# Kernel optimization log

Measured on AMD Instinct MI355X. Metric: run time of the kernel, lower is better.

## Reference

```python
import jax, jax.numpy as jnp
import numpy as np

N = 12        # ALL_QUBITS
COM_Q = 9     # COM_QUBITS
IMG_Q = 11    # IMG_QUBITS
LAYERS = 2
SQRT2 = float(np.sqrt(2.0))
H_GATE = jnp.asarray([[1.0, 1.0], [1.0, -1.0]], dtype=jnp.complex64) / SQRT2


def _bitrev_perm(q):
    # column j of the wires-1..q subspace corresponds to param index bitrev(j)
    idx = np.arange(2 ** q)
    rev = np.zeros_like(idx)
    for bpos in range(q):
        rev |= ((idx >> bpos) & 1) << (q - 1 - bpos)
    return rev


def _apply_1q(state, U, w):
    # state: (B, 2^N) complex; apply 2x2 gate U on wire w (wire 0 = MSB)
    B = state.shape[0]
    s = state.reshape(B, 2 ** w, 2, -1)
    return jnp.einsum('ij,bpjq->bpiq', U, s).reshape(B, -1)


def _apply_cnot(state, c, t):
    B = state.shape[0]
    s = state.reshape((B,) + (2,) * N)
    s0 = jax.lax.slice_in_dim(s, 0, 1, axis=c + 1)
    s1 = jnp.flip(jax.lax.slice_in_dim(s, 1, 2, axis=c + 1), axis=t + 1)
    return jnp.concatenate([s0, s1], axis=c + 1).reshape(B, -1)


def _frqi(state, angles, q):
    # Hadamards on wires 1..q, then uniformly-controlled RY(angles) on wire 0
    for w in range(1, q + 1):
        state = _apply_1q(state, H_GATE, w)
    rev = _bitrev_perm(q)
    half = 0.5 * angles[:, rev]            # (B, 2^q), angle per control column
    c = jnp.cos(half)[:, :, None]
    s = jnp.sin(half)[:, :, None]
    B = state.shape[0]
    st = state.reshape(B, 2, 2 ** q, -1)   # (B, wire0, wires1..q, rest)
    new0 = c * st[:, 0] - s * st[:, 1]
    new1 = s * st[:, 0] + c * st[:, 1]
    return jnp.stack([new0, new1], axis=1).reshape(B, -1)


def _rot(phi, theta, omega):
    # PennyLane Rot = RZ(omega) RY(theta) RZ(phi)
    c = jnp.cos(theta / 2)
    s = jnp.sin(theta / 2)
    m00 = jnp.exp(-0.5j * (phi + omega)) * c
    m01 = -jnp.exp(0.5j * (phi - omega)) * s
    m10 = jnp.exp(-0.5j * (phi - omega)) * s
    m11 = jnp.exp(0.5j * (phi + omega)) * c
    return jnp.stack([jnp.stack([m00, m01]), jnp.stack([m10, m11])])


def _circuit(com_params, img_params, qp):
    B = com_params.shape[0]
    state = jnp.zeros((B, 2 ** N), jnp.complex64).at[:, 0].set(1.0)
    state = _frqi(state, com_params, COM_Q)
    for l in range(LAYERS):  # StronglyEntanglingLayers
        for w in range(N):
            state = _apply_1q(state, _rot(qp[l, w, 0], qp[l, w, 1], qp[l, w, 2]), w)
        r = l % (N - 1) + 1  # default ranges
        for w in range(N):
            state = _apply_cnot(state, w, (w + r) % N)
    state = _frqi(state, img_params, IMG_Q)
    p = (jnp.abs(state.reshape(B, 2, -1)) ** 2).sum(axis=2)  # (B, 2) wire-0 probs
    return p[:, 1] - p[:, 0]  # expval of Hamiltonian = -1 * Z(0)


def setup_inputs() -> dict:
    key = jax.random.key(0)
    k1, k2, k3 = jax.random.split(key, 3)
    B = 1024
    x = jax.random.uniform(k1, (B, 2, 32, 32), dtype=jnp.float32)
    W = jax.random.normal(k2, (512, 2048), dtype=jnp.float32) * 0.02
    b = jnp.zeros((512,), dtype=jnp.float32)
    quantum_params = jax.random.uniform(k3, (LAYERS, N, 3), dtype=jnp.float32) * float(np.pi)
    return {"x": x, "W": W, "b": b, "quantum_params": quantum_params}


def reference(x, W, b, quantum_params):
    B = x.shape[0]
    xf = x.reshape(B, -1)                 # (B, 2048) img_params
    com = xf @ W.T + b                    # (B, 512) classical_nn output
    return _circuit(com, xf, quantum_params)
```

## Files before the change

kernel.cpp:

```cpp
#include <hip/hip_runtime.h>
#include <hip/hip_bf16.h>
#include <math.h>

#define RS2f 0.70710678118654752f

typedef __attribute__((ext_vector_type(8))) short bf16x8;
typedef __attribute__((ext_vector_type(4))) float f32x4;

__device__ __forceinline__ float bf2f(unsigned short h) {
    return __uint_as_float(((unsigned)h) << 16);
}
__device__ __forceinline__ ushort2 pk2(float a, float b) {
    union { __hip_bfloat162 h; ushort2 s; } u;
    u.h = __float22bfloat162_rn(make_float2(a, b));
    return u.s;
}

__global__ __launch_bounds__(256) void gemm_fused(const float* __restrict__ A,
                                                  const float* __restrict__ B,
                                                  float* __restrict__ P, int nch) {
    __shared__ short As[64 * 136];
    __shared__ short Bs[64 * 136];
    const int tid = threadIdx.x, lane = tid & 63, wv = tid >> 6;
    const int quad = lane >> 4, mrow = lane & 15;
    const int bid = blockIdx.x;
    const int xcd = bid & 7;
    const int idx = bid >> 3;
    const int mt  = ((xcd >> 1) << 2) | (idx & 3);
    const int nt  = ((xcd & 1) << 2) | ((idx >> 2) & 3);
    const int zt  = idx >> 4;
    const int m0 = mt * 64, n0 = nt * 64;
    const int kb = zt * nch * 64;
    const int srow = tid >> 2;
    const int sc = (tid & 3) * 16;

    f32x4 acc[4];
    #pragma unroll
    for (int j = 0; j < 4; ++j) acc[j] = (f32x4){0.f, 0.f, 0.f, 0.f};

    const float* Arow = A + (size_t)(m0 + srow) * 2048 + kb + sc;
    const float* Brow = B + (size_t)(n0 + srow) * 2048 + kb + sc;

    float4 av[4], bv[4];
    #pragma unroll
    for (int i = 0; i < 4; ++i) { av[i] = *(const float4*)(Arow + 4*i);
                                  bv[i] = *(const float4*)(Brow + 4*i); }

    for (int ch = 0; ch < nch; ++ch) {
        __syncthreads();
        #pragma unroll
        for (int i = 0; i < 4; ++i) {
            ushort2 h0 = pk2(av[i].x, av[i].y);
            ushort2 h1 = pk2(av[i].z, av[i].w);
            ushort2 l0 = pk2(av[i].x - bf2f(h0.x), av[i].y - bf2f(h0.y));
            ushort2 l1 = pk2(av[i].z - bf2f(h1.x), av[i].w - bf2f(h1.y));
            *(ushort4*)&As[srow * 136 + sc + 4*i]      = make_ushort4(h0.x, h0.y, h1.x, h1.y);
            *(ushort4*)&As[srow * 136 + 64 + sc + 4*i] = make_ushort4(l0.x, l0.y, l1.x, l1.y);
            h0 = pk2(bv[i].x, bv[i].y);
            h1 = pk2(bv[i].z, bv[i].w);
            l0 = pk2(bv[i].x - bf2f(h0.x), bv[i].y - bf2f(h0.y));
            l1 = pk2(bv[i].z - bf2f(h1.x), bv[i].w - bf2f(h1.y));
            *(ushort4*)&Bs[srow * 136 + sc + 4*i]      = make_ushort4(h0.x, h0.y, h1.x, h1.y);
            *(ushort4*)&Bs[srow * 136 + 64 + sc + 4*i] = make_ushort4(l0.x, l0.y, l1.x, l1.y);
        }
        __syncthreads();
        if (ch + 1 < nch) {
            const int o = (ch + 1) * 64;
            #pragma unroll
            for (int i = 0; i < 4; ++i) { av[i] = *(const float4*)(Arow + o + 4*i);
                                          bv[i] = *(const float4*)(Brow + o + 4*i); }
        }
        #pragma unroll
        for (int s = 0; s < 4; ++s) {
            const int off = s * 32 + quad * 8;
            bf16x8 af = *(const bf16x8*)&As[(wv * 16 + mrow) * 136 + off];
            #pragma unroll
            for (int j = 0; j < 4; ++j) {
                bf16x8 bf = *(const bf16x8*)&Bs[(j * 16 + mrow) * 136 + off];
                acc[j] = __builtin_amdgcn_mfma_f32_16x16x32_bf16(af, bf, acc[j], 0, 0, 0);
            }
        }
    }
    float* Pz = P + (size_t)zt * 524288;
    #pragma unroll
    for (int j = 0; j < 4; ++j)
        #pragma unroll
        for (int r = 0; r < 4; ++r)
            Pz[(m0 + wv * 16 + quad * 4 + r) * 512 + n0 + j * 16 + mrow] = acc[j][r];
}

__global__ __launch_bounds__(256) void reduce_kernel(float* __restrict__ P,
                                                     const float* __restrict__ bias,
                                                     int SK) {
    int i = blockIdx.x * 256 + threadIdx.x;
    float s = bias[i & 511];
    for (int z = 0; z < SK; ++z) s += P[(size_t)z * 524288 + i];
    P[i] = s;
}

__global__ __launch_bounds__(256) void gemm_f32(const float* __restrict__ A,
                                                const float* __restrict__ W,
                                                float* __restrict__ C) {
    __shared__ float Asf[64][33];
    __shared__ float Bsf[32][33];
    const int tid = threadIdx.x;
    const int m0 = blockIdx.x * 64;
    const int n0 = blockIdx.y * 32;
    const int tm = tid >> 4, tn = tid & 15;
    float acc[4][2] = {};
    for (int k0 = 0; k0 < 2048; k0 += 32) {
        #pragma unroll
        for (int i = 0; i < 8; ++i) {
            int idx = tid + i * 256;
            Asf[idx >> 5][idx & 31] = A[(m0 + (idx >> 5)) * 2048 + k0 + (idx & 31)];
        }
        #pragma unroll
        for (int i = 0; i < 4; ++i) {
            int idx = tid + i * 256;
            Bsf[idx >> 5][idx & 31] = W[(n0 + (idx >> 5)) * 2048 + k0 + (idx & 31)];
        }
        __syncthreads();
        #pragma unroll
        for (int kk = 0; kk < 32; ++kk) {
            float a0 = Asf[tm*4+0][kk], a1 = Asf[tm*4+1][kk];
            float a2 = Asf[tm*4+2][kk], a3 = Asf[tm*4+3][kk];
            float b0 = Bsf[tn*2+0][kk], b1 = Bsf[tn*2+1][kk];
            acc[0][0] += a0*b0; acc[0][1] += a0*b1;
            acc[1][0] += a1*b0; acc[1][1] += a1*b1;
            acc[2][0] += a2*b0; acc[2][1] += a2*b1;
            acc[3][0] += a3*b0; acc[3][1] += a3*b1;
        }
        __syncthreads();
    }
    #pragma unroll
    for (int r = 0; r < 4; ++r)
        #pragma unroll
        for (int c = 0; c < 2; ++c)
            C[(m0 + tm*4 + r) * 512 + n0 + tn*2 + c] = acc[r][c];
}

struct CMat { float m00r,m00i,m01r,m01i,m10r,m10i,m11r,m11i; };

__device__ __forceinline__ CMat mk_rot(const float* __restrict__ qp, int l, int w) {
    const float* g = qp + (l * 12 + w) * 3;
    float phi = g[0], th = g[1], om = g[2];
    float st, ct, sa, ca, sb, cb;
    sincosf(0.5f * th, &st, &ct);
    sincosf(0.5f * (phi + om), &sa, &ca);
    sincosf(0.5f * (phi - om), &sb, &cb);
    CMat M;
    M.m00r =  ct * ca; M.m00i = -ct * sa;
    M.m01r = -st * cb; M.m01i = -st * sb;
    M.m10r =  st * cb; M.m10i = -st * sb;
    M.m11r =  ct * ca; M.m11i =  ct * sa;
    return M;
}

template<int W> struct WI {
    static constexpr int kind = (W == 0 || W == 7) ? 2 : ((W >= 1 && W <= 6) ? 1 : 0);
    static constexpr int eb   = (W >= 8) ? (11 - W) : 0;
    static constexpr int lm   = (W >= 1 && W <= 6) ? (1 << (6 - W)) : 0;
    static constexpr int vm   = (W == 0) ? 2 : ((W == 7) ? 1 : 0);
};

__device__ __forceinline__ void exch_put(float* xbuf, int slot,
                                         const float vr[16], const float vi[16]) {
    __syncthreads();
    float4* p = (float4*)xbuf;
    #pragma unroll
    for (int j = 0; j < 8; ++j)
        p[(j << 8) + slot] = make_float4(vr[2*j], vi[2*j], vr[2*j+1], vi[2*j+1]);
    __syncthreads();
}

__device__ __forceinline__ void shfl_perm(float vr[16], float vi[16], int src) {
    #pragma unroll
    for (int e = 0; e < 16; ++e) {
        vr[e] = __shfl(vr[e], src, 64);
        vi[e] = __shfl(vi[e], src, 64);
    }
}

template<int EB>
__device__ __forceinline__ void rot_local(float vr[16], float vi[16], const CMat& M) {
    #pragma unroll
    for (int e = 0; e < 16; ++e) if (!(e & (1 << EB))) {
        const int e1 = e | (1 << EB);
        float x0r = vr[e],  x0i = vi[e];
        float x1r = vr[e1], x1i = vi[e1];
        vr[e]  = M.m00r*x0r - M.m00i*x0i + M.m01r*x1r - M.m01i*x1i;
        vi[e]  = M.m00r*x0i + M.m00i*x0r + M.m01r*x1i + M.m01i*x1r;
        vr[e1] = M.m10r*x0r - M.m10i*x0i + M.m11r*x1r - M.m11i*x1i;
        vi[e1] = M.m10r*x0i + M.m10i*x0r + M.m11r*x1i + M.m11i*x1r;
    }
}

template<int LM>
__device__ __forceinline__ void rot_lane(float vr[16], float vi[16], int lane, const CMat& M) {
    const bool hi = lane & LM;
    const float Ar = hi ? M.m11r : M.m00r, Ai = hi ? M.m11i : M.m00i;
    const float Br = hi ? M.m10r : M.m01r, Bi = hi ? M.m10i : M.m01i;
    #pragma unroll
    for (int e = 0; e < 16; ++e) {
        float pr = __shfl_xor(vr[e], LM, 64);
        float pi = __shfl_xor(vi[e], LM, 64);
        float orr = vr[e], oi = vi[e];
        vr[e] = Ar*orr - Ai*oi + Br*pr - Bi*pi;
        vi[e] = Ar*oi + Ai*orr + Br*pi + Bi*pr;
    }
}

template<int VM>
__device__ __forceinline__ void rot_wave(float vr[16], float vi[16], float* xbuf,
                                         int waveId, int lane, const CMat& M) {
    exch_put(xbuf, (waveId << 6) + lane, vr, vi);
    const float4* p = (const float4*)xbuf;
    const int ps = ((waveId ^ VM) << 6) + lane;
    const bool hi = waveId & VM;
    const float Ar = hi ? M.m11r : M.m00r, Ai = hi ? M.m11i : M.m00i;
    const float Br = hi ? M.m10r : M.m01r, Bi = hi ? M.m10i : M.m01i;
    #pragma unroll
    for (int j = 0; j < 8; ++j) {
        float4 q = p[(j << 8) + ps];
        const int e0 = 2*j, e1 = 2*j + 1;
        float r0 = vr[e0], i0 = vi[e0], r1 = vr[e1], i1 = vi[e1];
        vr[e0] = Ar*r0 - Ai*i0 + Br*q.x - Bi*q.y;
        vi[e0] = Ar*i0 + Ai*r0 + Br*q.y + Bi*q.x;
        vr[e1] = Ar*r1 - Ai*i1 + Br*q.z - Bi*q.w;
        vi[e1] = Ar*i1 + Ai*r1 + Br*q.w + Bi*q.z;
    }
}

template<int W>
__device__ __forceinline__ void rot_wire(float vr[16], float vi[16], float* xbuf,
                                         int waveId, int lane, const CMat& M) {
    if constexpr (WI<W>::kind == 0)      rot_local<WI<W>::eb>(vr, vi, M);
    else if constexpr (WI<W>::kind == 1) rot_lane<WI<W>::lm>(vr, vi, lane, M);
    else                                 rot_wave<WI<W>::vm>(vr, vi, xbuf, waveId, lane, M);
}

template<int C, int T>
__device__ __forceinline__ void cnot(float vr[16], float vi[16], float* xbuf,
                                     int waveId, int lane) {
    constexpr int ck = WI<C>::kind, tk = WI<T>::kind;
    if constexpr (ck == 0 && tk == 0) {
        constexpr int cb = 1 << WI<C>::eb, tb = 1 << WI<T>::eb;
        #pragma unroll
        for (int e = 0; e < 16; ++e) if ((e & cb) && !(e & tb)) {
            const int e1 = e | tb;
            float t = vr[e]; vr[e] = vr[e1]; vr[e1] = t;
            t = vi[e]; vi[e] = vi[e1]; vi[e1] = t;
        }
    } else if constexpr (ck == 0 && tk == 1) {
        constexpr int cb = 1 << WI<C>::eb, tm = WI<T>::lm;
        #pragma unroll
        for (int e = 0; e < 16; ++e) if (e & cb) {
            vr[e] = __shfl_xor(vr[e], tm, 64);
            vi[e] = __shfl_xor(vi[e], tm, 64);
        }
    } else if constexpr (ck == 0 && tk == 2) {
        constexpr int cb = 1 << WI<C>::eb, vm = WI<T>::vm;
        exch_put(xbuf, (waveId << 6) + lane, vr, vi);
        const float4* p = (const float4*)xbuf;
        const int ps = ((waveId ^ vm) << 6) + lane;
        #pragma unroll
        for (int j = 0; j < 8; ++j) {
            if ((((2*j) & cb) != 0) || (((2*j+1) & cb) != 0)) {
                float4 q = p[(j << 8) + ps];
                if (((2*j) & cb) != 0)   { vr[2*j]   = q.x; vi[2*j]   = q.y; }
                if (((2*j+1) & cb) != 0) { vr[2*j+1] = q.z; vi[2*j+1] = q.w; }
            }
        }
    } else if constexpr (ck == 1 && tk == 0) {
        constexpr int cm = WI<C>::lm, tb = 1 << WI<T>::eb;
        const bool cc = lane & cm;
        #pragma unroll
        for (int e = 0; e < 16; ++e) if (!(e & tb)) {
            const int e1 = e | tb;
            float a = vr[e], bb = vr[e1];
            vr[e] = cc ? bb : a; vr[e1] = cc ? a : bb;
            a = vi[e]; bb = vi[e1];
            vi[e] = cc ? bb : a; vi[e1] = cc ? a : bb;
        }
    } else if constexpr (ck == 1 && tk == 1) {
        constexpr int cm = WI<C>::lm, tm = WI<T>::lm;
        const int src = (lane & cm) ? (lane ^ tm) : lane;
        shfl_perm(vr, vi, src);
    } else if constexpr (ck == 1 && tk == 2) {
        constexpr int cm = WI<C>::lm, vm = WI<T>::vm;
        exch_put(xbuf, (waveId << 6) + lane, vr, vi);
        const float4* p = (const float4*)xbuf;
        const int ps = ((waveId ^ vm) << 6) + lane;
        const bool take = lane & cm;
        #pragma unroll
        for (int j = 0; j < 8; ++j) {
            float4 q = p[(j << 8) + ps];
            vr[2*j]   = take ? q.x : vr[2*j];   vi[2*j]   = take ? q.y : vi[2*j];
            vr[2*j+1] = take ? q.z : vr[2*j+1]; vi[2*j+1] = take ? q.w : vi[2*j+1];
        }
    } else if constexpr (ck == 2 && tk == 0) {
        constexpr int vm = WI<C>::vm, tb = 1 << WI<T>::eb;
        if (waveId & vm) {
            #pragma unroll
            for (int e = 0; e < 16; ++e) if (!(e & tb)) {
                const int e1 = e | tb;
                float t = vr[e]; vr[e] = vr[e1]; vr[e1] = t;
                t = vi[e]; vi[e] = vi[e1]; vi[e1] = t;
            }
        }
    } else {
        constexpr int vm = WI<C>::vm, tm = WI<T>::lm;
        if (waveId & vm) {
            #pragma unroll
            for (int e = 0; e < 16; ++e) {
                vr[e] = __shfl_xor(vr[e], tm, 64);
                vi[e] = __shfl_xor(vi[e], tm, 64);
            }
        }
    }
}

template<int W>
__device__ __forceinline__ void h_wire(float vr[16], float vi[16], float* xbuf,
                                       int waveId, int lane) {
    if constexpr (WI<W>::kind == 0) {
        constexpr int tb = 1 << WI<W>::eb;
        #pragma unroll
        for (int e = 0; e < 16; ++e) if (!(e & tb)) {
            const int e1 = e | tb;
            float x0 = vr[e], x1 = vr[e1];
            vr[e] = (x0 + x1) * RS2f; vr[e1] = (x0 - x1) * RS2f;
            x0 = vi[e]; x1 = vi[e1];
            vi[e] = (x0 + x1) * RS2f; vi[e1] = (x0 - x1) * RS2f;
        }
    } else if constexpr (WI<W>::kind == 1) {
        constexpr int m = WI<W>::lm;
        const float sgn = (lane & m) ? -RS2f : RS2f;
        #pragma unroll
        for (int e = 0; e < 16; ++e) {
            float pr = __shfl_xor(vr[e], m, 64);
            float pi = __shfl_xor(vi[e], m, 64);
            vr[e] = pr * RS2f + vr[e] * sgn;
            vi[e] = pi * RS2f + vi[e] * sgn;
        }
    } else {
        constexpr int vm = WI<W>::vm;
        exch_put(xbuf, (waveId << 6) + lane, vr, vi);
        const float4* p = (const float4*)xbuf;
        const int ps = ((waveId ^ vm) << 6) + lane;
        const float sgn = (waveId & vm) ? -RS2f : RS2f;
        #pragma unroll
        for (int j = 0; j < 8; ++j) {
            float4 q = p[(j << 8) + ps];
            vr[2*j]   = q.x * RS2f + vr[2*j]   * sgn;
            vi[2*j]   = q.y * RS2f + vi[2*j]   * sgn;
            vr[2*j+1] = q.z * RS2f + vr[2*j+1] * sgn;
            vi[2*j+1] = q.w * RS2f + vi[2*j+1] * sgn;
        }
    }
}

__global__ __launch_bounds__(256) void circuit_sa(const float* __restrict__ com,
                                                  const float* __restrict__ xf,
                                                  const float* __restrict__ qp,
                                                  float* __restrict__ out) {
    __shared__ float xbuf[8192];
    __shared__ float ang[2048];
    __shared__ CMat cms[24];
    const int tid = threadIdx.x, lane = tid & 63, waveId = tid >> 6;
    const int b = blockIdx.x;
    if (tid < 128) ((float4*)ang)[tid] = ((const float4*)(com + b * 512))[tid];
    if (tid >= 128 && tid < 152) {
        const int t = tid - 128;
        cms[t] = mk_rot(qp, t / 12, t % 12);
    }
    __syncthreads();
    float vr[16], vi[16];
    #pragma unroll
    for (int e = 0; e < 16; ++e) { vr[e] = 0.0f; vi[e] = 0.0f; }
    const float K9 = 0.044194173824159216f;
    #pragma unroll
    for (int m = 0; m < 4; ++m) {
        int j = (lane << 3) | ((waveId & 1) << 2) | m;
        int rj = (int)(__brev((unsigned)j) >> 23);
        float h = 0.5f * ang[rj];
        float s = __sinf(h), c = __cosf(h);
        vr[m << 2] = K9 * ((waveId & 2) ? s : c);
    }
    #pragma unroll 1
    for (int l = 0; l < 2; ++l) {
        const CMat* cl = &cms[l * 12];
        rot_wire<0 >(vr, vi, xbuf, waveId, lane, cl[0]);
        rot_wire<1 >(vr, vi, xbuf, waveId, lane, cl[1]);
        rot_wire<2 >(vr, vi, xbuf, waveId, lane, cl[2]);
        rot_wire<3 >(vr, vi, xbuf, waveId, lane, cl[3]);
        rot_wire<4 >(vr, vi, xbuf, waveId, lane, cl[4]);
        rot_wire<5 >(vr, vi, xbuf, waveId, lane, cl[5]);
        rot_wire<6 >(vr, vi, xbuf, waveId, lane, cl[6]);
        rot_wire<7 >(vr, vi, xbuf, waveId, lane, cl[7]);
        rot_wire<8 >(vr, vi, xbuf, waveId, lane, cl[8]);
        rot_wire<9 >(vr, vi, xbuf, waveId, lane, cl[9]);
        rot_wire<10>(vr, vi, xbuf, waveId, lane, cl[10]);
        rot_wire<11>(vr, vi, xbuf, waveId, lane, cl[11]);
        if (l == 0) {
            int j = lane;
            j ^= (j & 2)  ? 1  : 0;
            j ^= (j & 4)  ? 2  : 0;
            j ^= (j & 8)  ? 4  : 0;
            j ^= (j & 16) ? 8  : 0;
            j ^= (j & 32) ? 16 : 0;
            j ^= (waveId & 2) ? 32 : 0;
            shfl_perm(vr, vi, j);
            cnot<6,7>(vr,vi,xbuf,waveId,lane);   cnot<7,8>(vr,vi,xbuf,waveId,lane);
            cnot<8,9>(vr,vi,xbuf,waveId,lane);   cnot<9,10>(vr,vi,xbuf,waveId,lane);
            cnot<10,11>(vr,vi,xbuf,waveId,lane); cnot<11,0>(vr,vi,xbuf,waveId,lane);
        } else {
            int j = lane;
            j ^= (j & 4)  ? 1  : 0;
            j ^= (j & 8)  ? 2  : 0;
            j ^= (j & 16) ? 4  : 0;
            j ^= (j & 32) ? 8  : 0;
            j ^= (waveId & 2) ? 16 : 0;
            shfl_perm(vr, vi, j);
            cnot<5,7>(vr,vi,xbuf,waveId,lane);   cnot<6,8>(vr,vi,xbuf,waveId,lane);
            cnot<7,9>(vr,vi,xbuf,waveId,lane);   cnot<8,10>(vr,vi,xbuf,waveId,lane);
            cnot<9,11>(vr,vi,xbuf,waveId,lane);  cnot<10,0>(vr,vi,xbuf,waveId,lane);
            cnot<11,1>(vr,vi,xbuf,waveId,lane);
        }
    }
    h_wire<1>(vr,vi,xbuf,waveId,lane);  h_wire<2>(vr,vi,xbuf,waveId,lane);
    h_wire<3>(vr,vi,xbuf,waveId,lane);  h_wire<4>(vr,vi,xbuf,waveId,lane);
    h_wire<5>(vr,vi,xbuf,waveId,lane);  h_wire<6>(vr,vi,xbuf,waveId,lane);
    h_wire<7>(vr,vi,xbuf,waveId,lane);  h_wire<8>(vr,vi,xbuf,waveId,lane);
    h_wire<9>(vr,vi,xbuf,waveId,lane);  h_wire<10>(vr,vi,xbuf,waveId,lane);
    h_wire<11>(vr,vi,xbuf,waveId,lane);
    {
        const float4* x4 = (const float4*)(xf + b * 2048);
        ((float4*)ang)[tid]       = x4[tid];
        ((float4*)ang)[tid + 256] = x4[tid + 256];
    }
    __syncthreads();
    exch_put(xbuf, (waveId << 6) + lane, vr, vi);
    {
        const float4* p = (const float4*)xbuf;
        const int ps = ((waveId ^ 2) << 6) + lane;
        const bool hi = waveId & 2;
        float acc = 0.0f;
        #pragma unroll
        for (int j = 0; j < 8; ++j) {
            float4 q = p[(j << 8) + ps];
            #pragma unroll
            for (int h = 0; h < 2; ++h) {
                const int e = 2*j + h;
                const float prr = h ? q.z : q.x;
                const float pii = h ? q.w : q.y;
                int v = (lane << 5) | ((waveId & 1) << 4) | e;
                int rv = (int)(__brev((unsigned)v) >> 21);
                float ha = 0.5f * ang[rv];
                float s = __sinf(ha), c = __cosf(ha);
                float nr = hi ? (s*prr + c*vr[e]) : (c*vr[e] - s*prr);
                float ni = hi ? (s*pii + c*vi[e]) : (c*vi[e] - s*pii);
                acc += nr*nr + ni*ni;
            }
        }
        if (!hi) acc = -acc;
        #pragma unroll
        for (int off = 32; off > 0; off >>= 1) acc += __shfl_down(acc, off, 64);
        __syncthreads();
        if (lane == 0) xbuf[waveId] = acc;
        __syncthreads();
        if (tid == 0) out[b] = xbuf[0] + xbuf[1] + xbuf[2] + xbuf[3];
    }
}

extern "C" void kernel_launch(void* const* d_in, const int* in_sizes, int n_in,
                              void* d_out, int out_size, void* d_ws, size_t ws_size,
                              hipStream_t stream) {
    const float* x    = (const float*)d_in[0];
    const float* W    = (const float*)d_in[1];
    const float* bias = (const float*)d_in[2];
    const float* qp   = (const float*)d_in[3];
    float* out = (float*)d_out;

    const size_t SLAB = 2097152;
    float* P = (float*)d_ws;
    if (ws_size >= 2 * SLAB) {
        int SK = 2;
        if      (ws_size >= 8 * SLAB) SK = 8;
        else if (ws_size >= 4 * SLAB) SK = 4;
        gemm_fused<<<dim3(128 * SK), 256, 0, stream>>>(x, W, P, 32 / SK);
        reduce_kernel<<<2048, 256, 0, stream>>>(P, bias, SK);
        circuit_sa<<<1024, 256, 0, stream>>>(P, x, qp, out);
    } else {
        dim3 g(16, 16);
        gemm_f32<<<g, 256, 0, stream>>>(x, W, P);
        reduce_kernel<<<2048, 256, 0, stream>>>(P, bias, 1);
        circuit_sa<<<1024, 256, 0, stream>>>(P, x, qp, out);
    }
}
```

Measured before the change: 144.3 us.

## Pre-split operands into bf16 hi/lo and run a simpler split-K MFMA GEMM

```diff
diff --git a/kernel.cpp b/kernel.cpp
--- a/kernel.cpp
+++ b/kernel.cpp
@@ -5,6 +5,7 @@
 #define RS2f 0.70710678118654752f
 
 typedef __attribute__((ext_vector_type(8))) short bf16x8;
+typedef __attribute__((ext_vector_type(8))) unsigned short u16x8;
 typedef __attribute__((ext_vector_type(4))) float f32x4;
 
 __device__ __forceinline__ float bf2f(unsigned short h) {
@@ -14,6 +15,80 @@
     union { __hip_bfloat162 h; ushort2 s; } u;
     u.h = __float22bfloat162_rn(make_float2(a, b));
     return u.s;
+}
+
+__global__ __launch_bounds__(256) void convert_hl(const float* __restrict__ A,
+                                                  const float* __restrict__ B,
+                                                  unsigned short* __restrict__ Abf,
+                                                  unsigned short* __restrict__ Bbf) {
+    const int f = blockIdx.x * 256 + threadIdx.x;
+    const bool isA = f < 524288;
+    const float* src = isA ? A : B;
+    unsigned short* dst = isA ? Abf : Bbf;
+    const int g = isA ? f : f - 524288;
+    const int row = g >> 9, c4 = g & 511;
+    float4 v = *(const float4*)(src + ((size_t)g << 2));
+    ushort2 h0 = pk2(v.x, v.y), h1 = pk2(v.z, v.w);
+    ushort2 l0 = pk2(v.x - bf2f(h0.x), v.y - bf2f(h0.y));
+    ushort2 l1 = pk2(v.z - bf2f(h1.x), v.w - bf2f(h1.y));
+    unsigned short* o = dst + (size_t)row * 4096 + c4 * 4;
+    *(ushort4*)o          = make_ushort4(h0.x, h0.y, h1.x, h1.y);
+    *(ushort4*)(o + 2048) = make_ushort4(l0.x, l0.y, l1.x, l1.y);
+}
+
+__global__ __launch_bounds__(256) void gemm_bf(const unsigned short* __restrict__ Abf,
+                                               const unsigned short* __restrict__ Bbf,
+                                               float* __restrict__ P) {
+    __shared__ short As[64 * 68];
+    __shared__ short Bs[64 * 68];
+    const int tid = threadIdx.x, lane = tid & 63, wv = tid >> 6;
+    const int quad = lane >> 4, mrow = lane & 15;
+    const int bid = blockIdx.x;
+    const int zt  = bid & 7;
+    const int idx = bid >> 3;
+    const int mt  = idx >> 3, nt = idx & 7;
+    const int m0 = mt * 64, n0 = nt * 64;
+    const int row = tid >> 2, cg = tid & 3;
+
+    const unsigned short* Ar = Abf + (size_t)(m0 + row) * 4096 + zt * 512 + cg * 8;
+    const unsigned short* Br = Bbf + (size_t)(n0 + row) * 4096 + zt * 512 + cg * 8;
+
+    f32x4 acc[4];
+    #pragma unroll
+    for (int j = 0; j < 4; ++j) acc[j] = (f32x4){0.f, 0.f, 0.f, 0.f};
+
+    u16x8 a0 = *(const u16x8*)(Ar),      a1 = *(const u16x8*)(Ar + 32);
+    u16x8 b0 = *(const u16x8*)(Br),      b1 = *(const u16x8*)(Br + 32);
+
+    for (int s = 0; s < 8; ++s) {
+        __syncthreads();
+        *(u16x8*)&As[row * 68 + cg * 8]      = a0;
+        *(u16x8*)&As[row * 68 + 32 + cg * 8] = a1;
+        *(u16x8*)&Bs[row * 68 + cg * 8]      = b0;
+        *(u16x8*)&Bs[row * 68 + 32 + cg * 8] = b1;
+        __syncthreads();
+        if (s + 1 < 8) {
+            const int o = (s + 1) * 64;
+            a0 = *(const u16x8*)(Ar + o); a1 = *(const u16x8*)(Ar + o + 32);
+            b0 = *(const u16x8*)(Br + o); b1 = *(const u16x8*)(Br + o + 32);
+        }
+        #pragma unroll
+        for (int seg = 0; seg < 2; ++seg) {
+            const int off = seg * 32 + quad * 8;
+            bf16x8 af = *(const bf16x8*)&As[(wv * 16 + mrow) * 68 + off];
+            #pragma unroll
+            for (int j = 0; j < 4; ++j) {
+                bf16x8 bf = *(const bf16x8*)&Bs[(j * 16 + mrow) * 68 + off];
+                acc[j] = __builtin_amdgcn_mfma_f32_16x16x32_bf16(af, bf, acc[j], 0, 0, 0);
+            }
+        }
+    }
+    float* Pz = P + (size_t)zt * 524288;
+    #pragma unroll
+    for (int j = 0; j < 4; ++j)
+        #pragma unroll
+        for (int r = 0; r < 4; ++r)
+            Pz[(m0 + wv * 16 + quad * 4 + r) * 512 + n0 + j * 16 + mrow] = acc[j][r];
 }
 
 __global__ __launch_bounds__(256) void gemm_fused(const float* __restrict__ A,
@@ -366,7 +441,7 @@
                                                   float* __restrict__ out) {
     __shared__ float xbuf[8192];
     __shared__ float ang[2048];
-    __shared__ CMat cms[24];
+    CMat* cms = (CMat*)&ang[512];
     const int tid = threadIdx.x, lane = tid & 63, waveId = tid >> 6;
     const int b = blockIdx.x;
     if (tid < 128) ((float4*)ang)[tid] = ((const float4*)(com + b * 512))[tid];
@@ -483,8 +558,18 @@
     float* out = (float*)d_out;
 
     const size_t SLAB = 2097152;
-    float* P = (float*)d_ws;
-    if (ws_size >= 2 * SLAB) {
+    const size_t CONV = 12u * 1024 * 1024;
+
+    if (ws_size >= CONV + 8 * SLAB) {
+        unsigned short* Abf = (unsigned short*)d_ws;
+        unsigned short* Bbf = Abf + (size_t)1024 * 4096;
+        float* P = (float*)((char*)d_ws + CONV);
+        convert_hl<<<3072, 256, 0, stream>>>(x, W, Abf, Bbf);
+        gemm_bf<<<1024, 256, 0, stream>>>(Abf, Bbf, P);
+        reduce_kernel<<<2048, 256, 0, stream>>>(P, bias, 8);
+        circuit_sa<<<1024, 256, 0, stream>>>(P, x, qp, out);
+    } else if (ws_size >= 2 * SLAB) {
+        float* P = (float*)d_ws;
         int SK = 2;
         if      (ws_size >= 8 * SLAB) SK = 8;
         else if (ws_size >= 4 * SLAB) SK = 4;
@@ -492,6 +577,7 @@
         reduce_kernel<<<2048, 256, 0, stream>>>(P, bias, SK);
         circuit_sa<<<1024, 256, 0, stream>>>(P, x, qp, out);
     } else {
+        float* P = (float*)d_ws;
         dim3 g(16, 16);
         gemm_f32<<<g, 256, 0, stream>>>(x, W, P);
         reduce_kernel<<<2048, 256, 0, stream>>>(P, bias, 1);
```

Result: slower. 148.1 us (+2.6%).

## Fuse split-K reduction into circuit kernel and precompute rotation matrices in GEMM

Applied to the files above, without the earlier changes.

```diff
diff --git a/kernel.cpp b/kernel.cpp
--- a/kernel.cpp
+++ b/kernel.cpp
@@ -16,14 +16,34 @@
     return u.s;
 }
 
+struct CMat { float m00r,m00i,m01r,m01i,m10r,m10i,m11r,m11i; };
+
+__device__ __forceinline__ CMat mk_rot(const float* __restrict__ qp, int l, int w) {
+    const float* g = qp + (l * 12 + w) * 3;
+    float phi = g[0], th = g[1], om = g[2];
+    float st, ct, sa, ca, sb, cb;
+    sincosf(0.5f * th, &st, &ct);
+    sincosf(0.5f * (phi + om), &sa, &ca);
+    sincosf(0.5f * (phi - om), &sb, &cb);
+    CMat M;
+    M.m00r =  ct * ca; M.m00i = -ct * sa;
+    M.m01r = -st * cb; M.m01i = -st * sb;
+    M.m10r =  st * cb; M.m10i = -st * sb;
+    M.m11r =  ct * ca; M.m11i =  ct * sa;
+    return M;
+}
+
 __global__ __launch_bounds__(256) void gemm_fused(const float* __restrict__ A,
                                                   const float* __restrict__ B,
-                                                  float* __restrict__ P, int nch) {
+                                                  float* __restrict__ P, int nch,
+                                                  const float* __restrict__ qp,
+                                                  CMat* __restrict__ cmg) {
     __shared__ short As[64 * 136];
     __shared__ short Bs[64 * 136];
     const int tid = threadIdx.x, lane = tid & 63, wv = tid >> 6;
     const int quad = lane >> 4, mrow = lane & 15;
     const int bid = blockIdx.x;
+    if (bid == 0 && tid < 24) cmg[tid] = mk_rot(qp, tid / 12, tid % 12);
     const int xcd = bid & 7;
     const int idx = bid >> 3;
     const int mt  = ((xcd >> 1) << 2) | (idx & 3);
@@ -89,21 +109,16 @@
             Pz[(m0 + wv * 16 + quad * 4 + r) * 512 + n0 + j * 16 + mrow] = acc[j][r];
 }
 
-__global__ __launch_bounds__(256) void reduce_kernel(float* __restrict__ P,
-                                                     const float* __restrict__ bias,
-                                                     int SK) {
-    int i = blockIdx.x * 256 + threadIdx.x;
-    float s = bias[i & 511];
-    for (int z = 0; z < SK; ++z) s += P[(size_t)z * 524288 + i];
-    P[i] = s;
-}
-
 __global__ __launch_bounds__(256) void gemm_f32(const float* __restrict__ A,
                                                 const float* __restrict__ W,
-                                                float* __restrict__ C) {
+                                                float* __restrict__ C,
+                                                const float* __restrict__ qp,
+                                                CMat* __restrict__ cmg) {
     __shared__ float Asf[64][33];
     __shared__ float Bsf[32][33];
     const int tid = threadIdx.x;
+    if (blockIdx.x == 0 && blockIdx.y == 0 && tid < 24)
+        cmg[tid] = mk_rot(qp, tid / 12, tid % 12);
     const int m0 = blockIdx.x * 64;
     const int n0 = blockIdx.y * 32;
     const int tm = tid >> 4, tn = tid & 15;
@@ -137,23 +152,6 @@
         #pragma unroll
         for (int c = 0; c < 2; ++c)
             C[(m0 + tm*4 + r) * 512 + n0 + tn*2 + c] = acc[r][c];
-}
-
-struct CMat { float m00r,m00i,m01r,m01i,m10r,m10i,m11r,m11i; };
-
-__device__ __forceinline__ CMat mk_rot(const float* __restrict__ qp, int l, int w) {
-    const float* g = qp + (l * 12 + w) * 3;
-    float phi = g[0], th = g[1], om = g[2];
-    float st, ct, sa, ca, sb, cb;
-    sincosf(0.5f * th, &st, &ct);
-    sincosf(0.5f * (phi + om), &sa, &ca);
-    sincosf(0.5f * (phi - om), &sb, &cb);
-    CMat M;
-    M.m00r =  ct * ca; M.m00i = -ct * sa;
-    M.m01r = -st * cb; M.m01i = -st * sb;
-    M.m10r =  st * cb; M.m10i = -st * sb;
-    M.m11r =  ct * ca; M.m11i =  ct * sa;
-    return M;
 }
 
 template<int W> struct WI {
@@ -360,19 +358,21 @@
     }
 }
 
-__global__ __launch_bounds__(256) void circuit_sa(const float* __restrict__ com,
-                                                  const float* __restrict__ xf,
-                                                  const float* __restrict__ qp,
-                                                  float* __restrict__ out) {
+__global__ __launch_bounds__(256, 5) void circuit_red(const float* __restrict__ P,
+                                                      const float* __restrict__ xf,
+                                                      const CMat* __restrict__ cmg,
+                                                      const float* __restrict__ bias,
+                                                      float* __restrict__ out, int SK) {
     __shared__ float xbuf[8192];
-    __shared__ float ang[2048];
-    __shared__ CMat cms[24];
     const int tid = threadIdx.x, lane = tid & 63, waveId = tid >> 6;
     const int b = blockIdx.x;
-    if (tid < 128) ((float4*)ang)[tid] = ((const float4*)(com + b * 512))[tid];
-    if (tid >= 128 && tid < 152) {
-        const int t = tid - 128;
-        cms[t] = mk_rot(qp, t / 12, t % 12);
+    {
+        float2 s = ((const float2*)bias)[tid];
+        for (int z = 0; z < SK; ++z) {
+            float2 q = ((const float2*)(P + (size_t)z * 524288 + (size_t)b * 512))[tid];
+            s.x += q.x; s.y += q.y;
+        }
+        ((float2*)xbuf)[tid] = s;
     }
     __syncthreads();
     float vr[16], vi[16];
@@ -383,25 +383,25 @@
     for (int m = 0; m < 4; ++m) {
         int j = (lane << 3) | ((waveId & 1) << 2) | m;
         int rj = (int)(__brev((unsigned)j) >> 23);
-        float h = 0.5f * ang[rj];
+        float h = 0.5f * xbuf[rj];
         float s = __sinf(h), c = __cosf(h);
         vr[m << 2] = K9 * ((waveId & 2) ? s : c);
     }
     #pragma unroll 1
     for (int l = 0; l < 2; ++l) {
-        const CMat* cl = &cms[l * 12];
-        rot_wire<0 >(vr, vi, xbuf, waveId, lane, cl[0]);
-        rot_wire<1 >(vr, vi, xbuf, waveId, lane, cl[1]);
-        rot_wire<2 >(vr, vi, xbuf, waveId, lane, cl[2]);
-        rot_wire<3 >(vr, vi, xbuf, waveId, lane, cl[3]);
-        rot_wire<4 >(vr, vi, xbuf, waveId, lane, cl[4]);
-        rot_wire<5 >(vr, vi, xbuf, waveId, lane, cl[5]);
-        rot_wire<6 >(vr, vi, xbuf, waveId, lane, cl[6]);
-        rot_wire<7 >(vr, vi, xbuf, waveId, lane, cl[7]);
-        rot_wire<8 >(vr, vi, xbuf, waveId, lane, cl[8]);
-        rot_wire<9 >(vr, vi, xbuf, waveId, lane, cl[9]);
-        rot_wire<10>(vr, vi, xbuf, waveId, lane, cl[10]);
-        rot_wire<11>(vr, vi, xbuf, waveId, lane, cl[11]);
+        const CMat* cl = cmg + l * 12;
+        { CMat M = cl[0];  rot_wire<0 >(vr, vi, xbuf, waveId, lane, M); }
+        { CMat M = cl[1];  rot_wire<1 >(vr, vi, xbuf, waveId, lane, M); }
+        { CMat M = cl[2];  rot_wire<2 >(vr, vi, xbuf, waveId, lane, M); }
+        { CMat M = cl[3];  rot_wire<3 >(vr, vi, xbuf, waveId, lane, M); }
+        { CMat M = cl[4];  rot_wire<4 >(vr, vi, xbuf, waveId, lane, M); }
+        { CMat M = cl[5];  rot_wire<5 >(vr, vi, xbuf, waveId, lane, M); }
+        { CMat M = cl[6];  rot_wire<6 >(vr, vi, xbuf, waveId, lane, M); }
+        { CMat M = cl[7];  rot_wire<7 >(vr, vi, xbuf, waveId, lane, M); }
+        { CMat M = cl[8];  rot_wire<8 >(vr, vi, xbuf, waveId, lane, M); }
+        { CMat M = cl[9];  rot_wire<9 >(vr, vi, xbuf, waveId, lane, M); }
+        { CMat M = cl[10]; rot_wire<10>(vr, vi, xbuf, waveId, lane, M); }
+        { CMat M = cl[11]; rot_wire<11>(vr, vi, xbuf, waveId, lane, M); }
         if (l == 0) {
             int j = lane;
             j ^= (j & 2)  ? 1  : 0;
@@ -434,14 +434,9 @@
     h_wire<7>(vr,vi,xbuf,waveId,lane);  h_wire<8>(vr,vi,xbuf,waveId,lane);
     h_wire<9>(vr,vi,xbuf,waveId,lane);  h_wire<10>(vr,vi,xbuf,waveId,lane);
     h_wire<11>(vr,vi,xbuf,waveId,lane);
-    {
-        const float4* x4 = (const float4*)(xf + b * 2048);
-        ((float4*)ang)[tid]       = x4[tid];
-        ((float4*)ang)[tid + 256] = x4[tid + 256];
-    }
-    __syncthreads();
     exch_put(xbuf, (waveId << 6) + lane, vr, vi);
     {
+        const float* xrow = xf + (size_t)b * 2048;
         const float4* p = (const float4*)xbuf;
         const int ps = ((waveId ^ 2) << 6) + lane;
         const bool hi = waveId & 2;
@@ -456,7 +451,7 @@
                 const float pii = h ? q.w : q.y;
                 int v = (lane << 5) | ((waveId & 1) << 4) | e;
                 int rv = (int)(__brev((unsigned)v) >> 21);
-                float ha = 0.5f * ang[rv];
+                float ha = 0.5f * xrow[rv];
                 float s = __sinf(ha), c = __cosf(ha);
                 float nr = hi ? (s*prr + c*vr[e]) : (c*vr[e] - s*prr);
                 float ni = hi ? (s*pii + c*vi[e]) : (c*vi[e] - s*pii);
@@ -483,18 +478,20 @@
     float* out = (float*)d_out;
 
     const size_t SLAB = 2097152;
+    const size_t CMSZ = 1024;
     float* P = (float*)d_ws;
-    if (ws_size >= 2 * SLAB) {
+
+    if (ws_size >= 2 * SLAB + CMSZ) {
         int SK = 2;
-        if      (ws_size >= 8 * SLAB) SK = 8;
-        else if (ws_size >= 4 * SLAB) SK = 4;
-        gemm_fused<<<dim3(128 * SK), 256, 0, stream>>>(x, W, P, 32 / SK);
-        reduce_kernel<<<2048, 256, 0, stream>>>(P, bias, SK);
-        circuit_sa<<<1024, 256, 0, stream>>>(P, x, qp, out);
+        if      (ws_size >= 8 * SLAB + CMSZ) SK = 8;
+        else if (ws_size >= 4 * SLAB + CMSZ) SK = 4;
+        CMat* cmg = (CMat*)((char*)d_ws + (size_t)SK * SLAB);
+        gemm_fused<<<dim3(128 * SK), 256, 0, stream>>>(x, W, P, 32 / SK, qp, cmg);
+        circuit_red<<<1024, 256, 0, stream>>>(P, x, cmg, bias, out, SK);
     } else {
+        CMat* cmg = (CMat*)((char*)d_ws + SLAB);
         dim3 g(16, 16);
-        gemm_f32<<<g, 256, 0, stream>>>(x, W, P);
-        reduce_kernel<<<2048, 256, 0, stream>>>(P, bias, 1);
-        circuit_sa<<<1024, 256, 0, stream>>>(P, x, qp, out);
-    }
-}
+        gemm_f32<<<g, 256, 0, stream>>>(x, W, P, qp, cmg);
+        circuit_red<<<1024, 256, 0, stream>>>(P, x, cmg, bias, out, 1);
+    }
+}
```

New measurement: 172.6 us. 19.6% more time.
